# Optimization experiments

Measured on AMD Instinct MI355X. Metric: run time of the kernel, lower is better.

Reference implementation:

```python
import jax, jax.numpy as jnp
import numpy as np

EMBED = 1024
HEADS = 16
HEAD_DIM = EMBED // HEADS


def setup_inputs() -> dict:
    key = jax.random.key(0)
    ks = jax.random.split(key, 7)
    B, Sd, Se = 4, 2048, 2048
    dec = jax.random.normal(ks[0], (B, Sd, EMBED), dtype=jnp.float32)
    enc = jax.random.normal(ks[1], (B, Se, EMBED), dtype=jnp.float32)
    scale = 1.0 / np.sqrt(EMBED)
    W_q = jax.random.normal(ks[2], (EMBED, EMBED), dtype=jnp.float32) * scale
    W_k = jax.random.normal(ks[3], (EMBED, EMBED), dtype=jnp.float32) * scale
    W_v = jax.random.normal(ks[4], (EMBED, EMBED), dtype=jnp.float32) * scale
    W_o = jax.random.normal(ks[5], (EMBED, EMBED), dtype=jnp.float32) * scale
    b_o = jax.random.normal(ks[6], (EMBED,), dtype=jnp.float32) * 0.01
    return {"decoder_input": dec, "encoder_output": enc,
            "W_q": W_q, "W_k": W_k, "W_v": W_v, "W_o": W_o, "b_o": b_o}


def reference(decoder_input, encoder_output, W_q, W_k, W_v, W_o, b_o):
    B, Sd, E = decoder_input.shape
    Se = encoder_output.shape[1]
    # projections (nn.Linear applies x @ W.T; here W is stored as [in, out])
    Q = (decoder_input @ W_q).reshape(B, Sd, HEADS, HEAD_DIM)
    K = (encoder_output @ W_k).reshape(B, Se, HEADS, HEAD_DIM)
    V = (encoder_output @ W_v).reshape(B, Se, HEADS, HEAD_DIM)
    # scores: [B, H, Sd, Se]
    scores = jnp.einsum('bqhd,bkhd->bhqk', Q, K) / jnp.sqrt(jnp.float32(HEAD_DIM))
    attn = jax.nn.softmax(scores, axis=-1)
    out = jnp.einsum('bhqk,bkhd->bqhd', attn, V).reshape(B, Sd, E)
    return out @ W_o + b_o
```

## Files before the change

### kernel.cpp

```cpp
#include <hip/hip_runtime.h>
#include <hip/hip_bf16.h>

namespace {

typedef __attribute__((ext_vector_type(8))) short bf16x8;
typedef __attribute__((ext_vector_type(4))) float f32x4;
typedef __attribute__((ext_vector_type(4))) unsigned u32x4v;

constexpr int BATCH = 4;
constexpr int SEQ   = 2048;
constexpr int EMB   = 1024;
constexpr int NH    = 16;
constexpr int HD    = 64;
constexpr int MTOT  = BATCH * SEQ;
constexpr float LOG2E = 1.44269504088896f;
constexpr float SOFTMAX_C = 16.0f;

__device__ __forceinline__ unsigned short f2bf(float x) {
    unsigned int u = __float_as_uint(x);
    u += 0x7fffu + ((u >> 16) & 1u);
    return (unsigned short)(u >> 16);
}

__device__ __forceinline__ void gl_lds16(const void* g, void* l) {
    __builtin_amdgcn_global_load_lds(
        (const __attribute__((address_space(1))) unsigned int*)g,
        (__attribute__((address_space(3))) unsigned int*)l, 16, 0, 0);
}

__global__ __launch_bounds__(256)
void prep(const float* __restrict__ dec, const float* __restrict__ enc,
          unsigned short* __restrict__ decb, unsigned short* __restrict__ encb,
          const float* __restrict__ W0, const float* __restrict__ W1,
          const float* __restrict__ W2, const float* __restrict__ W3,
          unsigned short* __restrict__ WtBase, float qscale)
{
    __shared__ __align__(16) unsigned short Ts[64][65];
    const int tid = threadIdx.x;
    const int bid = blockIdx.x;
    if (bid < 16384) {
        const int zz = bid >> 13;
        const int i = (bid & 8191) * 256 + tid;
        const float* src = zz ? enc : dec;
        unsigned short* dst = zz ? encb : decb;
        float4 v = ((const float4*)src)[i];
        ushort4 o;
        o.x = f2bf(v.x); o.y = f2bf(v.y); o.z = f2bf(v.z); o.w = f2bf(v.w);
        ((ushort4*)dst)[i] = o;
        return;
    }
    const int zid = bid - 16384;
    const int z = zid >> 8;
    const float* W = (z == 0) ? W0 : (z == 1) ? W1 : (z == 2) ? W2 : W3;
    unsigned short* Wt = WtBase + (size_t)z * EMB * EMB;
    const float scale = (z == 0) ? qscale : 1.0f;
    const int n0 = (zid & 15) * 64, k0 = ((zid >> 4) & 15) * 64;
    #pragma unroll
    for (int i = 0; i < 4; ++i) {
        int id = tid + i * 256;
        int r = id >> 4, q = id & 15;
        float4 v = *(const float4*)&W[(size_t)(k0 + r) * EMB + n0 + q * 4];
        Ts[q * 4 + 0][r] = f2bf(v.x * scale);
        Ts[q * 4 + 1][r] = f2bf(v.y * scale);
        Ts[q * 4 + 2][r] = f2bf(v.z * scale);
        Ts[q * 4 + 3][r] = f2bf(v.w * scale);
    }
    __syncthreads();
    #pragma unroll
    for (int i = 0; i < 4; ++i) {
        int id = tid + i * 256;
        int rn = id >> 4, q = id & 15;
        ushort4 o;
        o.x = Ts[rn][q * 4 + 0]; o.y = Ts[rn][q * 4 + 1];
        o.z = Ts[rn][q * 4 + 2]; o.w = Ts[rn][q * 4 + 3];
        *(ushort4*)&Wt[(size_t)(n0 + rn) * EMB + k0 + q * 4] = o;
    }
}

enum OutKind { OUT_BF16R, OUT_F32B, OUT_VTK };

template<int OK>
__device__ __forceinline__
void gemm_body(const unsigned short* __restrict__ A, const unsigned short* __restrict__ Bt,
               const float* __restrict__ bias, void* __restrict__ Cout,
               int m0, int n0, int N, int Kd)
{
    __shared__ __align__(16) unsigned short As[2][128 * 32];
    __shared__ __align__(16) unsigned short Bs[2][128 * 32];
    const int tid  = threadIdx.x;
    const int lane = tid & 63, wave = tid >> 6;
    const int g = lane >> 4, c = lane & 15;
    const int wm = (wave & 1) * 64, wn = (wave >> 1) * 64;

    const int r0 = tid >> 2, s = tid & 3;
    const int sg = s ^ ((r0 + (r0 >> 2)) & 3);
    const unsigned short* ga0 = A  + (size_t)(m0 + r0)      * Kd + sg * 8;
    const unsigned short* ga1 = A  + (size_t)(m0 + r0 + 64) * Kd + sg * 8;
    const unsigned short* gb0 = Bt + (size_t)(n0 + r0)      * Kd + sg * 8;
    const unsigned short* gb1 = Bt + (size_t)(n0 + r0 + 64) * Kd + sg * 8;
    const int lo0 = tid * 8, lo1 = (256 + tid) * 8;

    const int cs = (c + (c >> 2)) & 3;

    f32x4 acc[4][4];
    #pragma unroll
    for (int i = 0; i < 4; ++i)
        #pragma unroll
        for (int j = 0; j < 4; ++j) acc[i][j] = (f32x4)0.0f;

    gl_lds16(ga0, &As[0][lo0]); gl_lds16(ga1, &As[0][lo1]);
    gl_lds16(gb0, &Bs[0][lo0]); gl_lds16(gb1, &Bs[0][lo1]);
    ga0 += 32; ga1 += 32; gb0 += 32; gb1 += 32;
    __syncthreads();

    const int KT = Kd / 32;
    for (int kt = 0; kt < KT; kt += 2) {
        #pragma unroll
        for (int h2 = 0; h2 < 2; ++h2) {
            const int k = kt + h2;
            if (k + 1 < KT) {
                gl_lds16(ga0, &As[h2 ^ 1][lo0]); gl_lds16(ga1, &As[h2 ^ 1][lo1]);
                gl_lds16(gb0, &Bs[h2 ^ 1][lo0]); gl_lds16(gb1, &Bs[h2 ^ 1][lo1]);
                ga0 += 32; ga1 += 32; gb0 += 32; gb1 += 32;
            }
            bf16x8 af[4], bfr[4];
            #pragma unroll
            for (int mt = 0; mt < 4; ++mt)
                af[mt]  = *(const bf16x8*)&As[h2][(wm + mt * 16 + c) * 32 + (g ^ cs) * 8];
            #pragma unroll
            for (int nt = 0; nt < 4; ++nt)
                bfr[nt] = *(const bf16x8*)&Bs[h2][(wn + nt * 16 + c) * 32 + (g ^ cs) * 8];
            #pragma unroll
            for (int mt = 0; mt < 4; ++mt)
                #pragma unroll
                for (int nt = 0; nt < 4; ++nt) {
                    if (OK == OUT_VTK)
                        acc[mt][nt] = __builtin_amdgcn_mfma_f32_16x16x32_bf16(af[mt], bfr[nt], acc[mt][nt], 0, 0, 0);
                    else
                        acc[mt][nt] = __builtin_amdgcn_mfma_f32_16x16x32_bf16(bfr[nt], af[mt], acc[mt][nt], 0, 0, 0);
                }
            __syncthreads();
        }
    }

    if (OK == OUT_VTK) {
        unsigned short* Vt = (unsigned short*)Cout;
        #pragma unroll
        for (int mt = 0; mt < 4; ++mt) {
            int m  = m0 + wm + mt * 16 + 4 * g;
            int bb = m >> 11, sl = m & 2047;
            int sp = (sl & ~31) | (((sl >> 2) & 3) << 3) | (((sl >> 4) & 1) << 2);
            #pragma unroll
            for (int nt = 0; nt < 4; ++nt) {
                int np = n0 + wn + nt * 16 + c - 1024;
                ushort4 o;
                o.x = f2bf(acc[mt][nt][0]); o.y = f2bf(acc[mt][nt][1]);
                o.z = f2bf(acc[mt][nt][2]); o.w = f2bf(acc[mt][nt][3]);
                *(ushort4*)&Vt[((size_t)bb * 1024 + np) * SEQ + sp] = o;
            }
        }
        return;
    }

    if (OK == OUT_BF16R) {
        unsigned short* C = (unsigned short*)Cout;
        #pragma unroll
        for (int mt = 0; mt < 4; ++mt) {
            int m = m0 + wm + mt * 16 + c;
            #pragma unroll
            for (int nt = 0; nt < 4; ++nt) {
                int n = n0 + wn + nt * 16 + 4 * g;
                unsigned u0, u1;
                asm("v_cvt_pk_bf16_f32 %0, %1, %2" : "=v"(u0) : "v"(acc[mt][nt][0]), "v"(acc[mt][nt][1]));
                asm("v_cvt_pk_bf16_f32 %0, %1, %2" : "=v"(u1) : "v"(acc[mt][nt][2]), "v"(acc[mt][nt][3]));
                uint2 st; st.x = u0; st.y = u1;
                *(uint2*)&C[(size_t)m * N + n] = st;
            }
        }
        return;
    }

    {
        float* C = (float*)Cout;
        #pragma unroll
        for (int nt = 0; nt < 4; ++nt) {
            int n = n0 + wn + nt * 16 + 4 * g;
            float4 bv = *(const float4*)&bias[n];
            #pragma unroll
            for (int mt = 0; mt < 4; ++mt) {
                int m = m0 + wm + mt * 16 + c;
                float4 o;
                o.x = acc[mt][nt][0] + bv.x;
                o.y = acc[mt][nt][1] + bv.y;
                o.z = acc[mt][nt][2] + bv.z;
                o.w = acc[mt][nt][3] + bv.w;
                *(float4*)&C[(size_t)m * N + n] = o;
            }
        }
    }
}

__global__ __launch_bounds__(256)
void proj_fused(const unsigned short* __restrict__ decb, const unsigned short* __restrict__ encb,
                const unsigned short* __restrict__ WtBase,
                unsigned short* __restrict__ Qb, unsigned short* __restrict__ Kb,
                unsigned short* __restrict__ Vtg)
{
    const int fid = blockIdx.y * 24 + blockIdx.x;
    const int xcd = fid & 7, idx = fid >> 3;
    const int mt  = (xcd << 3) | (idx / 24);
    const int nt  = idx % 24;
    const int m0  = mt * 128;
    if (nt < 8) {
        gemm_body<OUT_BF16R>(decb, WtBase, nullptr, Qb, m0, nt * 128, EMB, EMB);
    } else if (nt < 16) {
        gemm_body<OUT_BF16R>(encb, WtBase + (size_t)EMB * EMB, nullptr, Kb,
                             m0, (nt - 8) * 128, EMB, EMB);
    } else {
        gemm_body<OUT_VTK>(encb, WtBase + (size_t)EMB * EMB, nullptr, Vtg,
                           m0, (nt - 8) * 128, 0, EMB);
    }
}

__global__ __launch_bounds__(256)
void proj_out(const unsigned short* __restrict__ Ob, const unsigned short* __restrict__ WoT,
              const float* __restrict__ bo, float* __restrict__ out)
{
    const int fid = blockIdx.y * 8 + blockIdx.x;
    const int xcd = fid & 7, idx = fid >> 3;
    const int mt  = (xcd << 3) | (idx >> 3);
    const int nt  = idx & 7;
    gemm_body<OUT_F32B>(Ob, WoT, bo, out, mt * 128, nt * 128, EMB, EMB);
}

__global__ __launch_bounds__(256)
void attn(const unsigned short* __restrict__ Q, const unsigned short* __restrict__ K,
          const unsigned short* __restrict__ Vt, unsigned short* __restrict__ O)
{
    __shared__ __align__(16) unsigned short Ks[2][64 * 64];
    __shared__ __align__(16) unsigned short Vs[2][64 * 64];

    const int tid  = threadIdx.x;
    const int lane = tid & 63, wave = tid >> 6;
    const int g = lane >> 4, c = lane & 15, c7 = c & 7;

    const int fid  = blockIdx.y * 32 + blockIdx.x;
    const int xcd  = fid & 7, idx = fid >> 3;
    const int bh   = (xcd << 3) | (idx >> 5);
    const int qblk = idx & 31;
    const int b = bh >> 4, h = bh & 15;
    const int qw = qblk * 64 + wave * 16;

    const unsigned short* Qp0 = Q + (size_t)(b * SEQ + qw + c) * EMB + h * HD;
    bf16x8 qb[2];
    qb[0] = *(const bf16x8*)(Qp0 + g * 8);
    qb[1] = *(const bf16x8*)(Qp0 + 32 + g * 8);

    const int r0 = tid >> 3, s8 = tid & 7;
    const int sg = s8 ^ (r0 & 7);
    const unsigned short* gK0 = K + ((size_t)b * SEQ + r0) * EMB + h * HD + sg * 8;
    const unsigned short* gK1 = gK0 + (size_t)32 * EMB;
    const unsigned short* gV0 = Vt + (size_t)bh * HD * SEQ + (size_t)r0 * SEQ + sg * 8;
    const unsigned short* gV1 = gV0 + (size_t)32 * SEQ;
    const int lo0 = tid * 8, lo1 = (256 + tid) * 8;

    f32x4 oac[4];
    #pragma unroll
    for (int dt = 0; dt < 4; ++dt) oac[dt] = (f32x4)0.0f;
    f32x4 lacc = (f32x4)0.0f;
    const f32x4 minit = {-SOFTMAX_C, -SOFTMAX_C, -SOFTMAX_C, -SOFTMAX_C};
    const short onebf = (short)0x3F80;
    const bf16x8 vones = {onebf, onebf, onebf, onebf, onebf, onebf, onebf, onebf};

    gl_lds16(gK0, &Ks[0][lo0]); gl_lds16(gK1, &Ks[0][lo1]);
    gl_lds16(gV0, &Vs[0][lo0]); gl_lds16(gV1, &Vs[0][lo1]);
    gK0 += (size_t)64 * EMB; gK1 += (size_t)64 * EMB; gV0 += 64; gV1 += 64;
    __syncthreads();

    constexpr int T = SEQ / 64;
    for (int t = 0; t < T; t += 2) {
        #pragma unroll
        for (int h2 = 0; h2 < 2; ++h2) {
            const int tt = t + h2;
            if (tt + 1 < T) {
                gl_lds16(gK0, &Ks[h2 ^ 1][lo0]); gl_lds16(gK1, &Ks[h2 ^ 1][lo1]);
                gl_lds16(gV0, &Vs[h2 ^ 1][lo0]); gl_lds16(gV1, &Vs[h2 ^ 1][lo1]);
                gK0 += (size_t)64 * EMB; gK1 += (size_t)64 * EMB;
                gV0 += 64;               gV1 += 64;
            }

            f32x4 st[4];
            __builtin_amdgcn_s_setprio(1);
            #pragma unroll
            for (int kt = 0; kt < 4; ++kt) {
                bf16x8 ka0 = *(const bf16x8*)&Ks[h2][(kt * 16 + c) * 64 + (g ^ c7) * 8];
                bf16x8 ka1 = *(const bf16x8*)&Ks[h2][(kt * 16 + c) * 64 + ((4 + g) ^ c7) * 8];
                st[kt] = __builtin_amdgcn_mfma_f32_16x16x32_bf16(ka0, qb[0], minit, 0, 0, 0);
                st[kt] = __builtin_amdgcn_mfma_f32_16x16x32_bf16(ka1, qb[1], st[kt], 0, 0, 0);
            }
            __builtin_amdgcn_s_setprio(0);

            bf16x8 pa[2];
            {
                unsigned uu[8];
                #pragma unroll
                for (int kt = 0; kt < 4; ++kt) {
                    float p0 = __builtin_amdgcn_exp2f(st[kt][0]);
                    float p1 = __builtin_amdgcn_exp2f(st[kt][1]);
                    float p2 = __builtin_amdgcn_exp2f(st[kt][2]);
                    float p3 = __builtin_amdgcn_exp2f(st[kt][3]);
                    asm("v_cvt_pk_bf16_f32 %0, %1, %2" : "=v"(uu[2 * kt])     : "v"(p0), "v"(p1));
                    asm("v_cvt_pk_bf16_f32 %0, %1, %2" : "=v"(uu[2 * kt + 1]) : "v"(p2), "v"(p3));
                }
                u32x4v w0 = {uu[0], uu[1], uu[2], uu[3]};
                u32x4v w1 = {uu[4], uu[5], uu[6], uu[7]};
                pa[0] = __builtin_bit_cast(bf16x8, w0);
                pa[1] = __builtin_bit_cast(bf16x8, w1);
            }

            __builtin_amdgcn_s_setprio(1);
            #pragma unroll
            for (int dt = 0; dt < 4; ++dt) {
                bf16x8 vb0 = *(const bf16x8*)&Vs[h2][(dt * 16 + c) * 64 + (g ^ c7) * 8];
                bf16x8 vb1 = *(const bf16x8*)&Vs[h2][(dt * 16 + c) * 64 + ((4 + g) ^ c7) * 8];
                oac[dt] = __builtin_amdgcn_mfma_f32_16x16x32_bf16(pa[0], vb0, oac[dt], 0, 0, 0);
                oac[dt] = __builtin_amdgcn_mfma_f32_16x16x32_bf16(pa[1], vb1, oac[dt], 0, 0, 0);
            }
            lacc = __builtin_amdgcn_mfma_f32_16x16x32_bf16(pa[0], vones, lacc, 0, 0, 0);
            lacc = __builtin_amdgcn_mfma_f32_16x16x32_bf16(pa[1], vones, lacc, 0, 0, 0);
            __builtin_amdgcn_s_setprio(0);

            __syncthreads();
        }
    }

    unsigned short* Op = O + (size_t)(b * SEQ + qw) * EMB + h * HD;
    #pragma unroll
    for (int r = 0; r < 4; ++r) {
        float linv = 1.0f / lacc[r];
        #pragma unroll
        for (int dt = 0; dt < 4; ++dt)
            Op[(size_t)(4 * g + r) * EMB + dt * 16 + c] = f2bf(oac[dt][r] * linv);
    }
}

}

extern "C" void kernel_launch(void* const* d_in, const int* in_sizes, int n_in,
                              void* d_out, int out_size, void* d_ws, size_t ws_size,
                              hipStream_t stream)
{
    const float* dec = (const float*)d_in[0];
    const float* enc = (const float*)d_in[1];
    const float* Wq  = (const float*)d_in[2];
    const float* Wk  = (const float*)d_in[3];
    const float* Wv  = (const float*)d_in[4];
    const float* Wo  = (const float*)d_in[5];
    const float* bo  = (const float*)d_in[6];
    float* out = (float*)d_out;

    const size_t BIG = (size_t)MTOT * EMB;
    const size_t SML = (size_t)EMB * EMB;
    unsigned short* decb = (unsigned short*)d_ws;
    unsigned short* encb = decb + BIG;
    unsigned short* WqT  = encb + BIG;
    unsigned short* WoT  = WqT + 3 * SML;
    unsigned short* Qb   = WqT + 4 * SML;
    unsigned short* Kb   = Qb + BIG;
    unsigned short* Vtg  = Kb + BIG;
    unsigned short* Ob   = Vtg + BIG;

    dim3 blk(256);

    prep<<<dim3(16384 + 1024), blk, 0, stream>>>(
        dec, enc, decb, encb, Wq, Wk, Wv, Wo, WqT, 0.125f * LOG2E);

    proj_fused<<<dim3(24, MTOT / 128), blk, 0, stream>>>(decb, encb, WqT, Qb, Kb, Vtg);

    attn<<<dim3(SEQ / 64, BATCH * NH), blk, 0, stream>>>(Qb, Kb, Vtg, Ob);

    proj_out<<<dim3(EMB / 128, MTOT / 128), blk, 0, stream>>>(Ob, WoT, bo, out);
}
```

Before: 312.3 us.

## Retile projection GEMMs to 128x256 with 512 threads and triple-buffered LDS pipeline

Both projection GEMMs now use 512-thread blocks (8 waves) over 128x256 output tiles, so each A tile loaded into LDS feeds twice as many columns. The single-step double buffer becomes a three-stage ring using explicit vmcnt waits and raw barriers, which keeps two loads in flight while the MFMAs run, and setprio raises wave priority around the MFMA block. Grids are flattened with a new XCD-aware tile mapping. In exchange, LDS use per block grows and there are fewer blocks, which may reduce occupancy and leave the last wave of blocks poorly balanced.

Result: slower. 320.4 us (+2.6%).

```diff
diff --git a/kernel.cpp b/kernel.cpp
--- a/kernel.cpp
+++ b/kernel.cpp
@@ -83,22 +83,23 @@
 __device__ __forceinline__
 void gemm_body(const unsigned short* __restrict__ A, const unsigned short* __restrict__ Bt,
                const float* __restrict__ bias, void* __restrict__ Cout,
-               int m0, int n0, int N, int Kd)
-{
-    __shared__ __align__(16) unsigned short As[2][128 * 32];
-    __shared__ __align__(16) unsigned short Bs[2][128 * 32];
+               int m0, int n0, int N)
+{
+    constexpr int Kd = 1024;
+    __shared__ __align__(16) unsigned short As[3][128 * 32];
+    __shared__ __align__(16) unsigned short Bs[3][256 * 32];
     const int tid  = threadIdx.x;
     const int lane = tid & 63, wave = tid >> 6;
     const int g = lane >> 4, c = lane & 15;
-    const int wm = (wave & 1) * 64, wn = (wave >> 1) * 64;
+    const int wm = (wave >> 2) * 64;
+    const int wn = (wave & 3) * 64;
 
     const int r0 = tid >> 2, s = tid & 3;
     const int sg = s ^ ((r0 + (r0 >> 2)) & 3);
-    const unsigned short* ga0 = A  + (size_t)(m0 + r0)      * Kd + sg * 8;
-    const unsigned short* ga1 = A  + (size_t)(m0 + r0 + 64) * Kd + sg * 8;
-    const unsigned short* gb0 = Bt + (size_t)(n0 + r0)      * Kd + sg * 8;
-    const unsigned short* gb1 = Bt + (size_t)(n0 + r0 + 64) * Kd + sg * 8;
-    const int lo0 = tid * 8, lo1 = (256 + tid) * 8;
+    const unsigned short* ga  = A  + (size_t)(m0 + r0)       * Kd + sg * 8;
+    const unsigned short* gb0 = Bt + (size_t)(n0 + r0)       * Kd + sg * 8;
+    const unsigned short* gb1 = Bt + (size_t)(n0 + 128 + r0) * Kd + sg * 8;
+    const int loA = tid * 8, loB0 = tid * 8, loB1 = (512 + tid) * 8;
 
     const int cs = (c + (c >> 2)) & 3;
 
@@ -108,40 +109,52 @@
         #pragma unroll
         for (int j = 0; j < 4; ++j) acc[i][j] = (f32x4)0.0f;
 
-    gl_lds16(ga0, &As[0][lo0]); gl_lds16(ga1, &As[0][lo1]);
-    gl_lds16(gb0, &Bs[0][lo0]); gl_lds16(gb1, &Bs[0][lo1]);
-    ga0 += 32; ga1 += 32; gb0 += 32; gb1 += 32;
-    __syncthreads();
-
-    const int KT = Kd / 32;
-    for (int kt = 0; kt < KT; kt += 2) {
-        #pragma unroll
-        for (int h2 = 0; h2 < 2; ++h2) {
-            const int k = kt + h2;
-            if (k + 1 < KT) {
-                gl_lds16(ga0, &As[h2 ^ 1][lo0]); gl_lds16(ga1, &As[h2 ^ 1][lo1]);
-                gl_lds16(gb0, &Bs[h2 ^ 1][lo0]); gl_lds16(gb1, &Bs[h2 ^ 1][lo1]);
-                ga0 += 32; ga1 += 32; gb0 += 32; gb1 += 32;
-            }
-            bf16x8 af[4], bfr[4];
-            #pragma unroll
-            for (int mt = 0; mt < 4; ++mt)
-                af[mt]  = *(const bf16x8*)&As[h2][(wm + mt * 16 + c) * 32 + (g ^ cs) * 8];
-            #pragma unroll
-            for (int nt = 0; nt < 4; ++nt)
-                bfr[nt] = *(const bf16x8*)&Bs[h2][(wn + nt * 16 + c) * 32 + (g ^ cs) * 8];
-            #pragma unroll
-            for (int mt = 0; mt < 4; ++mt)
-                #pragma unroll
-                for (int nt = 0; nt < 4; ++nt) {
-                    if (OK == OUT_VTK)
-                        acc[mt][nt] = __builtin_amdgcn_mfma_f32_16x16x32_bf16(af[mt], bfr[nt], acc[mt][nt], 0, 0, 0);
-                    else
-                        acc[mt][nt] = __builtin_amdgcn_mfma_f32_16x16x32_bf16(bfr[nt], af[mt], acc[mt][nt], 0, 0, 0);
-                }
-            __syncthreads();
-        }
-    }
+    gl_lds16(ga, &As[0][loA]); gl_lds16(gb0, &Bs[0][loB0]); gl_lds16(gb1, &Bs[0][loB1]);
+    ga += 32; gb0 += 32; gb1 += 32;
+    gl_lds16(ga, &As[1][loA]); gl_lds16(gb0, &Bs[1][loB0]); gl_lds16(gb1, &Bs[1][loB1]);
+    ga += 32; gb0 += 32; gb1 += 32;
+    asm volatile("s_waitcnt vmcnt(3)" ::: "memory");
+    __builtin_amdgcn_s_barrier();
+
+#define GSTEP(T, B, B2)                                                          \
+    {                                                                            \
+        if ((T) + 2 < 32) {                                                      \
+            gl_lds16(ga,  &As[B2][loA]);                                         \
+            gl_lds16(gb0, &Bs[B2][loB0]);                                        \
+            gl_lds16(gb1, &Bs[B2][loB1]);                                        \
+            ga += 32; gb0 += 32; gb1 += 32;                                      \
+        }                                                                        \
+        bf16x8 af[4], bfv[4];                                                    \
+        _Pragma("unroll")                                                        \
+        for (int mt = 0; mt < 4; ++mt)                                           \
+            af[mt] = *(const bf16x8*)&As[B][(wm + mt * 16 + c) * 32 + (g ^ cs) * 8]; \
+        _Pragma("unroll")                                                        \
+        for (int nt = 0; nt < 4; ++nt)                                           \
+            bfv[nt] = *(const bf16x8*)&Bs[B][(wn + nt * 16 + c) * 32 + (g ^ cs) * 8]; \
+        __builtin_amdgcn_s_setprio(1);                                           \
+        _Pragma("unroll")                                                        \
+        for (int mt = 0; mt < 4; ++mt)                                           \
+            _Pragma("unroll")                                                    \
+            for (int nt = 0; nt < 4; ++nt) {                                     \
+                if (OK == OUT_VTK)                                               \
+                    acc[mt][nt] = __builtin_amdgcn_mfma_f32_16x16x32_bf16(af[mt], bfv[nt], acc[mt][nt], 0, 0, 0); \
+                else                                                             \
+                    acc[mt][nt] = __builtin_amdgcn_mfma_f32_16x16x32_bf16(bfv[nt], af[mt], acc[mt][nt], 0, 0, 0); \
+            }                                                                    \
+        __builtin_amdgcn_s_setprio(0);                                           \
+        if ((T) + 2 < 32)      { asm volatile("s_waitcnt vmcnt(3)" ::: "memory"); } \
+        else if ((T) + 1 < 32) { asm volatile("s_waitcnt vmcnt(0)" ::: "memory"); } \
+        if ((T) + 1 < 32) __builtin_amdgcn_s_barrier();                          \
+    }
+
+    for (int t = 0; t < 30; t += 3) {
+        GSTEP(t,     0, 2);
+        GSTEP(t + 1, 1, 0);
+        GSTEP(t + 2, 2, 1);
+    }
+    GSTEP(30, 0, 2);
+    GSTEP(31, 1, 0);
+#undef GSTEP
 
     if (OK == OUT_VTK) {
         unsigned short* Vt = (unsigned short*)Cout;
@@ -152,7 +165,7 @@
             int sp = (sl & ~31) | (((sl >> 2) & 3) << 3) | (((sl >> 4) & 1) << 2);
             #pragma unroll
             for (int nt = 0; nt < 4; ++nt) {
-                int np = n0 + wn + nt * 16 + c - 1024;
+                int np = n0 + wn + nt * 16 + c;
                 ushort4 o;
                 o.x = f2bf(acc[mt][nt][0]); o.y = f2bf(acc[mt][nt][1]);
                 o.z = f2bf(acc[mt][nt][2]); o.w = f2bf(acc[mt][nt][3]);
@@ -200,37 +213,37 @@
     }
 }
 
-__global__ __launch_bounds__(256)
+__global__ __launch_bounds__(512, 4)
 void proj_fused(const unsigned short* __restrict__ decb, const unsigned short* __restrict__ encb,
                 const unsigned short* __restrict__ WtBase,
                 unsigned short* __restrict__ Qb, unsigned short* __restrict__ Kb,
                 unsigned short* __restrict__ Vtg)
 {
-    const int fid = blockIdx.y * 24 + blockIdx.x;
-    const int xcd = fid & 7, idx = fid >> 3;
-    const int mt  = (xcd << 3) | (idx / 24);
-    const int nt  = idx % 24;
-    const int m0  = mt * 128;
-    if (nt < 8) {
-        gemm_body<OUT_BF16R>(decb, WtBase, nullptr, Qb, m0, nt * 128, EMB, EMB);
-    } else if (nt < 16) {
-        gemm_body<OUT_BF16R>(encb, WtBase + (size_t)EMB * EMB, nullptr, Kb,
-                             m0, (nt - 8) * 128, EMB, EMB);
+    const int fid  = blockIdx.x;
+    const int xcd  = fid & 7, idx = fid >> 3;
+    const int nt   = idx >> 3;
+    const int msub = idx & 7;
+    const int m0   = (xcd * 8 + msub) * 128;
+    const size_t SML = (size_t)EMB * EMB;
+    if (nt < 4) {
+        gemm_body<OUT_BF16R>(decb, WtBase, nullptr, Qb, m0, nt * 256, EMB);
+    } else if (nt < 8) {
+        gemm_body<OUT_BF16R>(encb, WtBase + SML, nullptr, Kb, m0, (nt - 4) * 256, EMB);
     } else {
-        gemm_body<OUT_VTK>(encb, WtBase + (size_t)EMB * EMB, nullptr, Vtg,
-                           m0, (nt - 8) * 128, 0, EMB);
-    }
-}
-
-__global__ __launch_bounds__(256)
+        gemm_body<OUT_VTK>(encb, WtBase + 2 * SML, nullptr, Vtg, m0, (nt - 8) * 256, 0);
+    }
+}
+
+__global__ __launch_bounds__(512, 4)
 void proj_out(const unsigned short* __restrict__ Ob, const unsigned short* __restrict__ WoT,
               const float* __restrict__ bo, float* __restrict__ out)
 {
-    const int fid = blockIdx.y * 8 + blockIdx.x;
-    const int xcd = fid & 7, idx = fid >> 3;
-    const int mt  = (xcd << 3) | (idx >> 3);
-    const int nt  = idx & 7;
-    gemm_body<OUT_F32B>(Ob, WoT, bo, out, mt * 128, nt * 128, EMB, EMB);
+    const int fid  = blockIdx.x;
+    const int xcd  = fid & 7, idx = fid >> 3;
+    const int nt   = idx >> 3;
+    const int msub = idx & 7;
+    const int m0   = (xcd * 8 + msub) * 128;
+    gemm_body<OUT_F32B>(Ob, WoT, bo, out, m0, nt * 256, EMB);
 }
 
 __global__ __launch_bounds__(256)
@@ -370,14 +383,12 @@
     unsigned short* Vtg  = Kb + BIG;
     unsigned short* Ob   = Vtg + BIG;
 
-    dim3 blk(256);
-
-    prep<<<dim3(16384 + 1024), blk, 0, stream>>>(
+    prep<<<dim3(16384 + 1024), dim3(256), 0, stream>>>(
         dec, enc, decb, encb, Wq, Wk, Wv, Wo, WqT, 0.125f * LOG2E);
 
-    proj_fused<<<dim3(24, MTOT / 128), blk, 0, stream>>>(decb, encb, WqT, Qb, Kb, Vtg);
-
-    attn<<<dim3(SEQ / 64, BATCH * NH), blk, 0, stream>>>(Qb, Kb, Vtg, Ob);
-
-    proj_out<<<dim3(EMB / 128, MTOT / 128), blk, 0, stream>>>(Ob, WoT, bo, out);
-}
+    proj_fused<<<dim3(768), dim3(512), 0, stream>>>(decb, encb, WqT, Qb, Kb, Vtg);
+
+    attn<<<dim3(SEQ / 64, BATCH * NH), dim3(256), 0, stream>>>(Qb, Kb, Vtg, Ob);
+
+    proj_out<<<dim3(256), dim3(512), 0, stream>>>(Ob, WoT, bo, out);
+}
```
